# Optimization experiments

Hardware: AMD Instinct MI355X
Metric: run time of the kernel (lower is better)

The kernel has to match this reference:

```python
import jax, jax.numpy as jnp
import numpy as np

N_NODES = 100000
N_EDGES = 3200000
N_FEAT = 128
N_CLASSES = 8


def setup_inputs() -> dict:
    key = jax.random.key(0)
    ks = jax.random.split(key, 8)
    h = jax.random.normal(ks[0], (N_NODES, N_FEAT), dtype=jnp.float32)
    edge_index = jax.random.randint(ks[1], (2, N_EDGES), 0, N_NODES, dtype=jnp.int64)
    def lin(k, fi, fo):
        return jax.random.normal(k, (fi, fo), dtype=jnp.float32) / np.sqrt(fi)
    return {
        "h": h,
        "edge_index": edge_index,
        "W1": lin(ks[2], N_FEAT, 16), "b1": jnp.zeros((16,), jnp.float32),
        "W2": lin(ks[3], 16, 4),      "b2": jnp.zeros((4,), jnp.float32),
        "W3": lin(ks[4], 4, 2),      "b3": jnp.zeros((2,), jnp.float32),
        "Wc": lin(ks[5], 2, N_CLASSES), "bc": jnp.zeros((N_CLASSES,), jnp.float32),
    }


def _gcn_norm(edge_index, n_nodes):
    # PyG GCNConv: add self-loops, symmetric normalization deg^-1/2 A deg^-1/2
    loop = jnp.arange(n_nodes, dtype=edge_index.dtype)
    src = jnp.concatenate([edge_index[0], loop])  # [E+N]
    dst = jnp.concatenate([edge_index[1], loop])
    deg = jax.ops.segment_sum(jnp.ones_like(dst, dtype=jnp.float32), dst,
                              num_segments=n_nodes)
    dinv = jnp.where(deg > 0, jax.lax.rsqrt(deg), 0.0)
    norm = dinv[src] * dinv[dst]  # [E+N]
    return src, dst, norm


def _gcn_conv(x, W, b, src, dst, norm, n_nodes):
    xw = x @ W                                # [N, Fo] linear first (small Fo)
    msg = xw[src] * norm[:, None]             # gather + scale  [E+N, Fo]
    out = jax.ops.segment_sum(msg, dst, num_segments=n_nodes)  # scatter-add
    return out + b


def reference(h, edge_index, W1, b1, W2, b2, W3, b3, Wc, bc):
    n = h.shape[0]
    src, dst, norm = _gcn_norm(edge_index, n)
    h1 = jnp.tanh(_gcn_conv(h, W1, b1, src, dst, norm, n))
    h2 = jnp.tanh(_gcn_conv(h1, W2, b2, src, dst, norm, n))
    h3 = jnp.tanh(_gcn_conv(h2, W3, b3, src, dst, norm, n))
    out = h3 @ Wc + bc
    return (out, h3)
```

## Files before the change

### kernel.cpp

```cpp
#include <hip/hip_runtime.h>
#include <math.h>

#define N_NODES 100000
#define N_EDGES 3200000
#define NPB    256
#define NBUCK  ((N_NODES + NPB - 1) / NPB)
#define NBLKA  256
#define EPB    ((N_EDGES + NBLKA - 1) / NBLKA)
#define NB_BLK ((N_NODES + 255) / 256)

#define NEW_WS_WORDS (3u*N_NODES + N_EDGES + 3200000u + NBUCK*NBLKA + NBUCK + 2u)
#define NEW_WS_BYTES (NEW_WS_WORDS * 4u)
#define ATOMIC_WS_BYTES ((33u*N_NODES + 16u) * 4u)

__global__ void k_detect_i64(const int* __restrict__ ei_words, int* __restrict__ flag) {
    if (blockIdx.x == 0 && threadIdx.x == 0) {
        int allzero = 1;
        for (int i = 0; i < 64; i++)
            if (ei_words[2 * i + 1] != 0) allzero = 0;
        *flag = allzero;
    }
}

__device__ __forceinline__ unsigned load_idx(const int* p32, const long long* p64,
                                             int is64, int e) {
    return is64 ? (unsigned)(unsigned long long)p64[e] : (unsigned)p32[e];
}

__global__ __launch_bounds__(256) void k_bcount(const int* __restrict__ dst32,
                                                const long long* __restrict__ dst64,
                                                const int* __restrict__ flag,
                                                int* __restrict__ cmat) {
    __shared__ int lc[NBUCK];
    int t = threadIdx.x, blk = blockIdx.x;
    for (int i = t; i < NBUCK; i += 256) lc[i] = 0;
    __syncthreads();
    int is64 = *flag;
    int e0 = blk * EPB;
    int e1 = e0 + EPB; if (e1 > N_EDGES) e1 = N_EDGES;
    for (int e = e0 + t; e < e1; e += 256) {
        unsigned d = load_idx(dst32, dst64, is64, e);
        if (d < N_NODES) atomicAdd(&lc[d >> 8], 1);
    }
    __syncthreads();
    for (int b = t; b < NBUCK; b += 256) cmat[b * NBLKA + blk] = lc[b];
}

__global__ __launch_bounds__(256) void k_bsum(const int* __restrict__ cmat,
                                              int* __restrict__ bt) {
    int b = blockIdx.x, t = threadIdx.x;
    int v = cmat[b * NBLKA + t];
#pragma unroll
    for (int off = 32; off > 0; off >>= 1) v += __shfl_down(v, off, 64);
    __shared__ int s[4];
    if ((t & 63) == 0) s[t >> 6] = v;
    __syncthreads();
    if (t == 0) bt[b] = s[0] + s[1] + s[2] + s[3];
}

__global__ __launch_bounds__(512) void k_btscan(int* __restrict__ bt) {
    __shared__ int s[512];
    int t = threadIdx.x;
    s[t] = (t < NBUCK) ? bt[t] : 0;
    __syncthreads();
    for (int off = 1; off < 512; off <<= 1) {
        int v = (t >= off) ? s[t - off] : 0;
        __syncthreads();
        s[t] += v;
        __syncthreads();
    }
    if (t < NBUCK) bt[t] = (t == 0) ? 0 : s[t - 1];
    if (t == 0) bt[NBUCK] = s[NBUCK - 1];
}

__global__ __launch_bounds__(256) void k_boffs(int* __restrict__ cmat,
                                               const int* __restrict__ bt) {
    __shared__ int s[256];
    int b = blockIdx.x, t = threadIdx.x;
    int v0 = cmat[b * NBLKA + t];
    s[t] = v0;
    __syncthreads();
    for (int off = 1; off < 256; off <<= 1) {
        int v = (t >= off) ? s[t - off] : 0;
        __syncthreads();
        s[t] += v;
        __syncthreads();
    }
    cmat[b * NBLKA + t] = ((t == 0) ? 0 : s[t - 1]) + bt[b];
}

__global__ __launch_bounds__(256) void k_bscatter(const int* __restrict__ src32,
                                                  const long long* __restrict__ src64,
                                                  const int* __restrict__ dst32,
                                                  const long long* __restrict__ dst64,
                                                  const int* __restrict__ flag,
                                                  const int* __restrict__ cmat,
                                                  int* __restrict__ P) {
    __shared__ int cur[NBUCK];
    int t = threadIdx.x, blk = blockIdx.x;
    for (int i = t; i < NBUCK; i += 256) cur[i] = cmat[i * NBLKA + blk];
    __syncthreads();
    int is64 = *flag;
    int e0 = blk * EPB;
    int e1 = e0 + EPB; if (e1 > N_EDGES) e1 = N_EDGES;
    for (int e = e0 + t; e < e1; e += 256) {
        unsigned d = load_idx(dst32, dst64, is64, e);
        if (d < N_NODES) {
            unsigned s = load_idx(src32, src64, is64, e);
            int pos = atomicAdd(&cur[d >> 8], 1);
            P[pos] = (int)(((d & 255u) << 17) | (s & 0x1FFFFu));
        }
    }
}

__global__ __launch_bounds__(256) void k_bbuild(const int* __restrict__ P,
                                                const int* __restrict__ bt,
                                                int* __restrict__ adj,
                                                int* __restrict__ rowstart,
                                                int* __restrict__ rowend,
                                                float* __restrict__ dinv) {
    __shared__ int cnt[NPB];
    __shared__ int s[NPB];
    int b = blockIdx.x, t = threadIdx.x;
    int bo = bt[b], be = bt[b + 1];
    cnt[t] = 0;
    __syncthreads();
    for (int i = bo + t; i < be; i += 256) atomicAdd(&cnt[P[i] >> 17], 1);
    __syncthreads();
    s[t] = cnt[t];
    __syncthreads();
    for (int off = 1; off < 256; off <<= 1) {
        int v = (t >= off) ? s[t - off] : 0;
        __syncthreads();
        s[t] += v;
        __syncthreads();
    }
    int ex = (t == 0) ? 0 : s[t - 1];
    int node = b * NPB + t;
    if (node < N_NODES) {
        rowstart[node] = bo + ex;
        rowend[node]   = bo + ex + cnt[t];
        dinv[node]     = rsqrtf((float)cnt[t] + 1.0f);
    }
    __syncthreads();
    s[t] = ex;
    __syncthreads();
    for (int i = bo + t; i < be; i += 256) {
        int ent = P[i];
        int pos = bo + atomicAdd(&s[ent >> 17], 1);
        adj[pos] = ent & 0x1FFFF;
    }
}

__global__ __launch_bounds__(256) void k_gemm1(const float* __restrict__ h,
                                               const float* __restrict__ W,
                                               const float* __restrict__ dinv,
                                               float* __restrict__ xs,
                                               float* acc) {
    __shared__ float Wt[16 * 132];
    __shared__ float Hs[16 * 132];
    int tid = threadIdx.x;
    for (int i = tid; i < 2048; i += 256) {
        int k = i >> 4, f = i & 15;
        Wt[f * 132 + k] = W[i];
    }
    int nodeBase = blockIdx.x * 16;
    for (int i = tid; i < 512; i += 256) {
        int r = i >> 5, c = i & 31;
        float4 v = ((const float4*)(h + (size_t)(nodeBase + r) * 128))[c];
        *((float4*)&Hs[r * 132 + c * 4]) = v;
    }
    __syncthreads();
    int nl = tid >> 4;
    int f  = tid & 15;
    int n  = nodeBase + nl;
    const float* hr = &Hs[nl * 132];
    const float* wr = &Wt[f * 132];
    float s = 0.0f;
#pragma unroll
    for (int k = 0; k < 128; k++) s += hr[k] * wr[k];
    s *= dinv[n];
    xs[n * 16 + f]  = s;
    acc[n * 16 + f] = s;
}

template <int FI, int FO>
__global__ __launch_bounds__(256) void k_gemm_small(const float* __restrict__ x,
                                                    const float* __restrict__ W,
                                                    const float* __restrict__ dinv,
                                                    float* __restrict__ xs,
                                                    float* acc) {
    int i = blockIdx.x * 256 + threadIdx.x;
    if (i >= N_NODES * FO) return;
    int n = i / FO, f = i % FO;
    float s = 0.0f;
#pragma unroll
    for (int k = 0; k < FI; k++) s += x[n * FI + k] * W[k * FO + f];
    s *= dinv[n];
    xs[i] = s;
    acc[i] = s;
}

template <int F, int NL>
__global__ __launch_bounds__(256) void k_pull(const float* __restrict__ xs,
                                              const int* __restrict__ adj,
                                              const int* __restrict__ rowstart,
                                              const int* __restrict__ rowend,
                                              const float* __restrict__ dinv,
                                              const float* __restrict__ b,
                                              float* __restrict__ out) {
    constexpr int R = NL / F;
    int t = threadIdx.x;
    int g = t / NL, q = t % NL;
    int f = q % F,  k = q / F;
    int n = blockIdx.x * (256 / NL) + g;
    if (n >= N_NODES) return;
    int s0 = rowstart[n], e0 = rowend[n];
    float acc = 0.0f;
    for (int j = s0 + k; j < e0; j += R)
        acc += xs[adj[j] * F + f];
#pragma unroll
    for (int off = NL / 2; off >= F; off >>= 1)
        acc += __shfl_xor(acc, off, 64);
    if (k == 0) {
        acc += xs[n * F + f];
        out[n * F + f] = tanhf(dinv[n] * acc + b[f]);
    }
}

__global__ __launch_bounds__(256) void k_pull_final(const float* __restrict__ xs,
                                                    const int* __restrict__ adj,
                                                    const int* __restrict__ rowstart,
                                                    const int* __restrict__ rowend,
                                                    const float* __restrict__ dinv,
                                                    const float* __restrict__ b3,
                                                    const float* __restrict__ Wc,
                                                    const float* __restrict__ bc,
                                                    float* __restrict__ out,
                                                    float* __restrict__ h3out) {
    const int NL = 8;
    int t = threadIdx.x;
    int g = t / NL, q = t % NL;
    int f = q & 1, k = q >> 1;
    int n = blockIdx.x * (256 / NL) + g;
    if (n >= N_NODES) return;
    int s0 = rowstart[n], e0 = rowend[n];
    float acc = 0.0f;
    for (int j = s0 + k; j < e0; j += 4)
        acc += xs[adj[j] * 2 + f];
    acc += __shfl_xor(acc, 4, 64);
    acc += __shfl_xor(acc, 2, 64);
    float a = 0.0f;
    if (q < 2) {
        acc += xs[n * 2 + f];
        a = tanhf(dinv[n] * acc + b3[f]);
        h3out[2 * n + f] = a;
    }
    int wl = t & 63, gb = wl & ~7;
    float a0 = __shfl(a, gb, 64);
    float a1 = __shfl(a, gb + 1, 64);
    out[8 * n + q] = a0 * Wc[q] + a1 * Wc[8 + q] + bc[q];
}

template <int F>
__global__ __launch_bounds__(256) void k_scatter(const int* __restrict__ src32,
                                                 const long long* __restrict__ src64,
                                                 const int* __restrict__ dst32,
                                                 const long long* __restrict__ dst64,
                                                 const int* __restrict__ flag,
                                                 const float* __restrict__ xs,
                                                 float* __restrict__ acc) {
    long long gid = (long long)blockIdx.x * 256 + threadIdx.x;
    int e = (int)(gid / F), f = (int)(gid % F);
    if (e < N_EDGES) {
        int is64 = *flag;
        unsigned s = load_idx(src32, src64, is64, e);
        unsigned d = load_idx(dst32, dst64, is64, e);
        if (s < N_NODES && d < N_NODES)
            atomicAdd(&acc[d * F + f], xs[s * F + f]);
    }
}
__global__ __launch_bounds__(256) void k_deg_init(float* __restrict__ deg) {
    int i = blockIdx.x * 256 + threadIdx.x;
    if (i < N_NODES) deg[i] = 1.0f;
}
__global__ __launch_bounds__(256) void k_deg_count(const int* __restrict__ dst32,
                                                   const long long* __restrict__ dst64,
                                                   const int* __restrict__ flag,
                                                   float* __restrict__ deg) {
    int e = blockIdx.x * 256 + threadIdx.x;
    if (e < N_EDGES) {
        unsigned d = load_idx(dst32, dst64, *flag, e);
        if (d < N_NODES) atomicAdd(&deg[d], 1.0f);
    }
}
__global__ __launch_bounds__(256) void k_rsqrt(float* __restrict__ deg) {
    int i = blockIdx.x * 256 + threadIdx.x;
    if (i < N_NODES) deg[i] = rsqrtf(deg[i]);
}
template <int F>
__global__ __launch_bounds__(256) void k_finish(const float* __restrict__ acc,
                                                const float* __restrict__ dinv,
                                                const float* __restrict__ b,
                                                float* __restrict__ out) {
    int i = blockIdx.x * 256 + threadIdx.x;
    if (i >= N_NODES * F) return;
    int n = i / F, f = i % F;
    out[i] = tanhf(dinv[n] * acc[i] + b[f]);
}
__global__ __launch_bounds__(256) void k_final(const float* __restrict__ acc3,
                                               const float* __restrict__ dinv,
                                               const float* __restrict__ b3,
                                               const float* __restrict__ Wc,
                                               const float* __restrict__ bc,
                                               float* __restrict__ out,
                                               float* __restrict__ h3out) {
    int n = blockIdx.x * 256 + threadIdx.x;
    if (n >= N_NODES) return;
    float di = dinv[n];
    float a0 = tanhf(di * acc3[2 * n + 0] + b3[0]);
    float a1 = tanhf(di * acc3[2 * n + 1] + b3[1]);
    h3out[2 * n + 0] = a0;
    h3out[2 * n + 1] = a1;
#pragma unroll
    for (int c = 0; c < 8; c++)
        out[8 * n + c] = a0 * Wc[c] + a1 * Wc[8 + c] + bc[c];
}
__global__ __launch_bounds__(256) void k_zero_out(float* __restrict__ out, int n) {
    int i = blockIdx.x * 256 + threadIdx.x;
    if (i < n) out[i] = 0.0f;
}

extern "C" void kernel_launch(void* const* d_in, const int* in_sizes, int n_in,
                              void* d_out, int out_size, void* d_ws, size_t ws_size,
                              hipStream_t stream) {
    float* out = (float*)d_out;
    const float* h   = (const float*)d_in[0];
    const void*  ei  = d_in[1];
    const float* W1  = (const float*)d_in[2];
    const float* b1  = (const float*)d_in[3];
    const float* W2  = (const float*)d_in[4];
    const float* b2  = (const float*)d_in[5];
    const float* W3  = (const float*)d_in[6];
    const float* b3  = (const float*)d_in[7];
    const float* Wc  = (const float*)d_in[8];
    const float* bc  = (const float*)d_in[9];

    const int*       src32 = (const int*)ei;
    const int*       dst32 = src32 + N_EDGES;
    const long long* src64 = (const long long*)ei;
    const long long* dst64 = src64 + N_EDGES;

    float* h3out = out + 8 * N_NODES;
    const int NB_E = (N_EDGES + 255) / 256;

    if (d_ws != nullptr && ws_size >= NEW_WS_BYTES) {
        float* dinv    = (float*)d_ws;
        int* rowstart  = (int*)(dinv + N_NODES);
        int* rowend    = rowstart + N_NODES;
        int* adj       = rowend + N_NODES;
        int* S         = adj + N_EDGES;
        float* xs      = (float*)S;
        float* hbuf    = xs + 16 * N_NODES;
        int* P         = S;
        int* cmat      = S + 3200000;
        int* bt        = cmat + NBUCK * NBLKA;
        int* flag      = bt + NBUCK + 1;

        k_detect_i64<<<1, 64, 0, stream>>>(src32, flag);
        k_bcount<<<NBLKA, 256, 0, stream>>>(dst32, dst64, flag, cmat);
        k_bsum<<<NBUCK, 256, 0, stream>>>(cmat, bt);
        k_btscan<<<1, 512, 0, stream>>>(bt);
        k_boffs<<<NBUCK, 256, 0, stream>>>(cmat, bt);
        k_bscatter<<<NBLKA, 256, 0, stream>>>(src32, src64, dst32, dst64, flag, cmat, P);
        k_bbuild<<<NBUCK, 256, 0, stream>>>(P, bt, adj, rowstart, rowend, dinv);

        k_gemm1<<<N_NODES / 16, 256, 0, stream>>>(h, W1, dinv, xs, xs);
        k_pull<16, 64><<<(N_NODES * 64 + 255) / 256, 256, 0, stream>>>(
            xs, adj, rowstart, rowend, dinv, b1, hbuf);
        k_gemm_small<16, 4><<<(N_NODES * 4 + 255) / 256, 256, 0, stream>>>(hbuf, W2, dinv, xs, xs);
        k_pull<4, 16><<<(N_NODES * 16 + 255) / 256, 256, 0, stream>>>(
            xs, adj, rowstart, rowend, dinv, b2, hbuf);
        k_gemm_small<4, 2><<<(N_NODES * 2 + 255) / 256, 256, 0, stream>>>(hbuf, W3, dinv, xs, xs);
        k_pull_final<<<(N_NODES * 8 + 255) / 256, 256, 0, stream>>>(
            xs, adj, rowstart, rowend, dinv, b3, Wc, bc, out, h3out);
        return;
    }

    if (d_ws != nullptr && ws_size >= ATOMIC_WS_BYTES) {
        float* ws   = (float*)d_ws;
        float* dinv = ws;
        float* bufA = dinv + N_NODES;
        float* bufB = bufA + 16 * N_NODES;
        int*   flag = (int*)(bufB + 16 * N_NODES);
        float* xs1 = bufA, *acc1 = bufB, *h1 = bufA;
        float* xs2 = bufB, *acc2 = bufB + 4 * N_NODES, *h2 = bufA;
        float* xs3 = bufB, *acc3 = bufB + 2 * N_NODES;

        k_detect_i64<<<1, 64, 0, stream>>>(src32, flag);
        k_deg_init<<<NB_BLK, 256, 0, stream>>>(dinv);
        k_deg_count<<<NB_E, 256, 0, stream>>>(dst32, dst64, flag, dinv);
        k_rsqrt<<<NB_BLK, 256, 0, stream>>>(dinv);
        k_gemm1<<<N_NODES / 16, 256, 0, stream>>>(h, W1, dinv, xs1, acc1);
        k_scatter<16><<<(int)(((long long)N_EDGES * 16 + 255) / 256), 256, 0, stream>>>(
            src32, src64, dst32, dst64, flag, xs1, acc1);
        k_finish<16><<<(N_NODES * 16 + 255) / 256, 256, 0, stream>>>(acc1, dinv, b1, h1);
        k_gemm_small<16, 4><<<(N_NODES * 4 + 255) / 256, 256, 0, stream>>>(h1, W2, dinv, xs2, acc2);
        k_scatter<4><<<(int)(((long long)N_EDGES * 4 + 255) / 256), 256, 0, stream>>>(
            src32, src64, dst32, dst64, flag, xs2, acc2);
        k_finish<4><<<(N_NODES * 4 + 255) / 256, 256, 0, stream>>>(acc2, dinv, b2, h2);
        k_gemm_small<4, 2><<<(N_NODES * 2 + 255) / 256, 256, 0, stream>>>(h2, W3, dinv, xs3, acc3);
        k_scatter<2><<<(int)(((long long)N_EDGES * 2 + 255) / 256), 256, 0, stream>>>(
            src32, src64, dst32, dst64, flag, xs3, acc3);
        k_final<<<NB_BLK, 256, 0, stream>>>(acc3, dinv, b3, Wc, bc, out, h3out);
        return;
    }

    k_zero_out<<<(out_size + 255) / 256, 256, 0, stream>>>(out, out_size);
}
```

Baseline: 351.0 us.

## Split layer-1 features into two 8-wide halves, add nontemporal loads, double bucket blocks

Layer-1 features are stored as two planar 8-wide halves, and each half is aggregated in its own pull pass so the gather working set per pass is smaller and more cache-friendly. The layer-2 pull moves from 16 to 32 lanes per node. Nontemporal loads are used for edge indices, P, adj and h to avoid polluting cache with streamed data. The bucket-sort block count doubles to 512, and the scan kernels are adjusted to match. The split means adj is read twice for layer 1, and the extra pull launch adds overhead.

```diff
diff --git a/kernel.cpp b/kernel.cpp
--- a/kernel.cpp
+++ b/kernel.cpp
@@ -5,12 +5,14 @@
 #define N_EDGES 3200000
 #define NPB    256
 #define NBUCK  ((N_NODES + NPB - 1) / NPB)
-#define NBLKA  256
+#define NBLKA  512
 #define EPB    ((N_EDGES + NBLKA - 1) / NBLKA)
 #define NB_BLK ((N_NODES + 255) / 256)
 
-#define NEW_WS_WORDS (3u*N_NODES + N_EDGES + 3200000u + NBUCK*NBLKA + NBUCK + 2u)
-#define NEW_WS_BYTES (NEW_WS_WORDS * 4u)
+typedef float f4nt __attribute__((ext_vector_type(4)));
+
+#define MAIN_WS_WORDS (3u*N_NODES + N_EDGES + 3200000u + NBUCK*NBLKA + NBUCK + 2u)
+#define MAIN_WS_BYTES (MAIN_WS_WORDS * 4u)
 #define ATOMIC_WS_BYTES ((33u*N_NODES + 16u) * 4u)
 
 __global__ void k_detect_i64(const int* __restrict__ ei_words, int* __restrict__ flag) {
@@ -24,7 +26,8 @@
 
 __device__ __forceinline__ unsigned load_idx(const int* p32, const long long* p64,
                                              int is64, int e) {
-    return is64 ? (unsigned)(unsigned long long)p64[e] : (unsigned)p32[e];
+    return is64 ? (unsigned)(unsigned long long)__builtin_nontemporal_load(&p64[e])
+                : (unsigned)__builtin_nontemporal_load(&p32[e]);
 }
 
 __global__ __launch_bounds__(256) void k_bcount(const int* __restrict__ dst32,
@@ -36,8 +39,7 @@
     for (int i = t; i < NBUCK; i += 256) lc[i] = 0;
     __syncthreads();
     int is64 = *flag;
-    int e0 = blk * EPB;
-    int e1 = e0 + EPB; if (e1 > N_EDGES) e1 = N_EDGES;
+    int e0 = blk * EPB, e1 = e0 + EPB; if (e1 > N_EDGES) e1 = N_EDGES;
     for (int e = e0 + t; e < e1; e += 256) {
         unsigned d = load_idx(dst32, dst64, is64, e);
         if (d < N_NODES) atomicAdd(&lc[d >> 8], 1);
@@ -49,7 +51,7 @@
 __global__ __launch_bounds__(256) void k_bsum(const int* __restrict__ cmat,
                                               int* __restrict__ bt) {
     int b = blockIdx.x, t = threadIdx.x;
-    int v = cmat[b * NBLKA + t];
+    int v = cmat[b * NBLKA + t] + cmat[b * NBLKA + t + 256];
 #pragma unroll
     for (int off = 32; off > 0; off >>= 1) v += __shfl_down(v, off, 64);
     __shared__ int s[4];
@@ -73,14 +75,13 @@
     if (t == 0) bt[NBUCK] = s[NBUCK - 1];
 }
 
-__global__ __launch_bounds__(256) void k_boffs(int* __restrict__ cmat,
+__global__ __launch_bounds__(512) void k_boffs(int* __restrict__ cmat,
                                                const int* __restrict__ bt) {
-    __shared__ int s[256];
+    __shared__ int s[512];
     int b = blockIdx.x, t = threadIdx.x;
-    int v0 = cmat[b * NBLKA + t];
-    s[t] = v0;
-    __syncthreads();
-    for (int off = 1; off < 256; off <<= 1) {
+    s[t] = cmat[b * NBLKA + t];
+    __syncthreads();
+    for (int off = 1; off < 512; off <<= 1) {
         int v = (t >= off) ? s[t - off] : 0;
         __syncthreads();
         s[t] += v;
@@ -101,8 +102,7 @@
     for (int i = t; i < NBUCK; i += 256) cur[i] = cmat[i * NBLKA + blk];
     __syncthreads();
     int is64 = *flag;
-    int e0 = blk * EPB;
-    int e1 = e0 + EPB; if (e1 > N_EDGES) e1 = N_EDGES;
+    int e0 = blk * EPB, e1 = e0 + EPB; if (e1 > N_EDGES) e1 = N_EDGES;
     for (int e = e0 + t; e < e1; e += 256) {
         unsigned d = load_idx(dst32, dst64, is64, e);
         if (d < N_NODES) {
@@ -125,7 +125,8 @@
     int bo = bt[b], be = bt[b + 1];
     cnt[t] = 0;
     __syncthreads();
-    for (int i = bo + t; i < be; i += 256) atomicAdd(&cnt[P[i] >> 17], 1);
+    for (int i = bo + t; i < be; i += 256)
+        atomicAdd(&cnt[__builtin_nontemporal_load(&P[i]) >> 17], 1);
     __syncthreads();
     s[t] = cnt[t];
     __syncthreads();
@@ -146,17 +147,16 @@
     s[t] = ex;
     __syncthreads();
     for (int i = bo + t; i < be; i += 256) {
-        int ent = P[i];
+        int ent = __builtin_nontemporal_load(&P[i]);
         int pos = bo + atomicAdd(&s[ent >> 17], 1);
         adj[pos] = ent & 0x1FFFF;
     }
 }
 
-__global__ __launch_bounds__(256) void k_gemm1(const float* __restrict__ h,
-                                               const float* __restrict__ W,
-                                               const float* __restrict__ dinv,
-                                               float* __restrict__ xs,
-                                               float* acc) {
+__global__ __launch_bounds__(256) void k_gemm1_p(const float* __restrict__ h,
+                                                 const float* __restrict__ W,
+                                                 const float* __restrict__ dinv,
+                                                 float* __restrict__ xs) {
     __shared__ float Wt[16 * 132];
     __shared__ float Hs[16 * 132];
     int tid = threadIdx.x;
@@ -167,68 +167,64 @@
     int nodeBase = blockIdx.x * 16;
     for (int i = tid; i < 512; i += 256) {
         int r = i >> 5, c = i & 31;
-        float4 v = ((const float4*)(h + (size_t)(nodeBase + r) * 128))[c];
-        *((float4*)&Hs[r * 132 + c * 4]) = v;
-    }
-    __syncthreads();
-    int nl = tid >> 4;
-    int f  = tid & 15;
-    int n  = nodeBase + nl;
+        f4nt v = __builtin_nontemporal_load(
+            ((const f4nt*)(h + (size_t)(nodeBase + r) * 128)) + c);
+        *((f4nt*)&Hs[r * 132 + c * 4]) = v;
+    }
+    __syncthreads();
+    int nl = tid >> 4, f = tid & 15;
+    int n = nodeBase + nl;
     const float* hr = &Hs[nl * 132];
     const float* wr = &Wt[f * 132];
     float s = 0.0f;
 #pragma unroll
     for (int k = 0; k < 128; k++) s += hr[k] * wr[k];
     s *= dinv[n];
-    xs[n * 16 + f]  = s;
-    acc[n * 16 + f] = s;
+    xs[(f >> 3) * (8 * N_NODES) + n * 8 + (f & 7)] = s;
 }
 
 template <int FI, int FO>
-__global__ __launch_bounds__(256) void k_gemm_small(const float* __restrict__ x,
-                                                    const float* __restrict__ W,
-                                                    const float* __restrict__ dinv,
-                                                    float* __restrict__ xs,
-                                                    float* acc) {
+__global__ __launch_bounds__(256) void k_gemm_smallp(const float* __restrict__ x,
+                                                     const float* __restrict__ W,
+                                                     const float* __restrict__ dinv,
+                                                     float* __restrict__ xs) {
     int i = blockIdx.x * 256 + threadIdx.x;
     if (i >= N_NODES * FO) return;
     int n = i / FO, f = i % FO;
     float s = 0.0f;
 #pragma unroll
     for (int k = 0; k < FI; k++) s += x[n * FI + k] * W[k * FO + f];
-    s *= dinv[n];
-    xs[i] = s;
-    acc[i] = s;
-}
-
-template <int F, int NL>
-__global__ __launch_bounds__(256) void k_pull(const float* __restrict__ xs,
+    xs[i] = s * dinv[n];
+}
+
+template <int F, int NL, int FTOT, int FOFF>
+__global__ __launch_bounds__(256) void k_pull(const float* __restrict__ xsp,
                                               const int* __restrict__ adj,
                                               const int* __restrict__ rowstart,
                                               const int* __restrict__ rowend,
                                               const float* __restrict__ dinv,
-                                              const float* __restrict__ b,
+                                              const float* __restrict__ bias,
                                               float* __restrict__ out) {
     constexpr int R = NL / F;
     int t = threadIdx.x;
     int g = t / NL, q = t % NL;
-    int f = q % F,  k = q / F;
+    int f = q % F, k = q / F;
     int n = blockIdx.x * (256 / NL) + g;
     if (n >= N_NODES) return;
     int s0 = rowstart[n], e0 = rowend[n];
     float acc = 0.0f;
     for (int j = s0 + k; j < e0; j += R)
-        acc += xs[adj[j] * F + f];
+        acc += xsp[__builtin_nontemporal_load(&adj[j]) * F + f];
 #pragma unroll
     for (int off = NL / 2; off >= F; off >>= 1)
         acc += __shfl_xor(acc, off, 64);
     if (k == 0) {
-        acc += xs[n * F + f];
-        out[n * F + f] = tanhf(dinv[n] * acc + b[f]);
-    }
-}
-
-__global__ __launch_bounds__(256) void k_pull_final(const float* __restrict__ xs,
+        acc += xsp[n * F + f];
+        out[n * FTOT + FOFF + f] = tanhf(dinv[n] * acc + bias[f]);
+    }
+}
+
+__global__ __launch_bounds__(256) void k_pull_final(const float* __restrict__ xsp,
                                                     const int* __restrict__ adj,
                                                     const int* __restrict__ rowstart,
                                                     const int* __restrict__ rowend,
@@ -247,12 +243,12 @@
     int s0 = rowstart[n], e0 = rowend[n];
     float acc = 0.0f;
     for (int j = s0 + k; j < e0; j += 4)
-        acc += xs[adj[j] * 2 + f];
+        acc += xsp[__builtin_nontemporal_load(&adj[j]) * 2 + f];
     acc += __shfl_xor(acc, 4, 64);
     acc += __shfl_xor(acc, 2, 64);
     float a = 0.0f;
     if (q < 2) {
-        acc += xs[n * 2 + f];
+        acc += xsp[n * 2 + f];
         a = tanhf(dinv[n] * acc + b3[f]);
         h3out[2 * n + f] = a;
     }
@@ -262,6 +258,50 @@
     out[8 * n + q] = a0 * Wc[q] + a1 * Wc[8 + q] + bc[q];
 }
 
+__global__ __launch_bounds__(256) void k_gemm1(const float* __restrict__ h,
+                                               const float* __restrict__ W,
+                                               const float* __restrict__ dinv,
+                                               float* __restrict__ xs, float* acc) {
+    __shared__ float Wt[16 * 132];
+    __shared__ float Hs[16 * 132];
+    int tid = threadIdx.x;
+    for (int i = tid; i < 2048; i += 256) {
+        int k = i >> 4, f = i & 15;
+        Wt[f * 132 + k] = W[i];
+    }
+    int nodeBase = blockIdx.x * 16;
+    for (int i = tid; i < 512; i += 256) {
+        int r = i >> 5, c = i & 31;
+        float4 v = ((const float4*)(h + (size_t)(nodeBase + r) * 128))[c];
+        *((float4*)&Hs[r * 132 + c * 4]) = v;
+    }
+    __syncthreads();
+    int nl = tid >> 4, f = tid & 15;
+    int n = nodeBase + nl;
+    const float* hr = &Hs[nl * 132];
+    const float* wr = &Wt[f * 132];
+    float s = 0.0f;
+#pragma unroll
+    for (int k = 0; k < 128; k++) s += hr[k] * wr[k];
+    s *= dinv[n];
+    xs[n * 16 + f] = s;
+    acc[n * 16 + f] = s;
+}
+template <int FI, int FO>
+__global__ __launch_bounds__(256) void k_gemm_small(const float* __restrict__ x,
+                                                    const float* __restrict__ W,
+                                                    const float* __restrict__ dinv,
+                                                    float* __restrict__ xs, float* acc) {
+    int i = blockIdx.x * 256 + threadIdx.x;
+    if (i >= N_NODES * FO) return;
+    int n = i / FO, f = i % FO;
+    float s = 0.0f;
+#pragma unroll
+    for (int k = 0; k < FI; k++) s += x[n * FI + k] * W[k * FO + f];
+    s *= dinv[n];
+    xs[i] = s;
+    acc[i] = s;
+}
 template <int F>
 __global__ __launch_bounds__(256) void k_scatter(const int* __restrict__ src32,
                                                  const long long* __restrict__ src64,
@@ -354,35 +394,37 @@
     float* h3out = out + 8 * N_NODES;
     const int NB_E = (N_EDGES + 255) / 256;
 
-    if (d_ws != nullptr && ws_size >= NEW_WS_BYTES) {
-        float* dinv    = (float*)d_ws;
-        int* rowstart  = (int*)(dinv + N_NODES);
-        int* rowend    = rowstart + N_NODES;
-        int* adj       = rowend + N_NODES;
-        int* S         = adj + N_EDGES;
-        float* xs      = (float*)S;
-        float* hbuf    = xs + 16 * N_NODES;
-        int* P         = S;
-        int* cmat      = S + 3200000;
-        int* bt        = cmat + NBUCK * NBLKA;
-        int* flag      = bt + NBUCK + 1;
+    if (d_ws != nullptr && ws_size >= MAIN_WS_BYTES) {
+        float* dinv   = (float*)d_ws;
+        int* rowstart = (int*)(dinv + N_NODES);
+        int* rowend   = rowstart + N_NODES;
+        int* adj      = rowend + N_NODES;
+        int* S        = adj + N_EDGES;
+        float* xs     = (float*)S;
+        float* hbuf   = xs + 16 * N_NODES;
+        int* P        = S;
+        int* cmat     = S + 3200000;
+        int* bt       = cmat + NBUCK * NBLKA;
+        int* flag     = bt + NBUCK + 1;
 
         k_detect_i64<<<1, 64, 0, stream>>>(src32, flag);
         k_bcount<<<NBLKA, 256, 0, stream>>>(dst32, dst64, flag, cmat);
         k_bsum<<<NBUCK, 256, 0, stream>>>(cmat, bt);
         k_btscan<<<1, 512, 0, stream>>>(bt);
-        k_boffs<<<NBUCK, 256, 0, stream>>>(cmat, bt);
+        k_boffs<<<NBUCK, 512, 0, stream>>>(cmat, bt);
         k_bscatter<<<NBLKA, 256, 0, stream>>>(src32, src64, dst32, dst64, flag, cmat, P);
         k_bbuild<<<NBUCK, 256, 0, stream>>>(P, bt, adj, rowstart, rowend, dinv);
 
-        k_gemm1<<<N_NODES / 16, 256, 0, stream>>>(h, W1, dinv, xs, xs);
-        k_pull<16, 64><<<(N_NODES * 64 + 255) / 256, 256, 0, stream>>>(
+        k_gemm1_p<<<N_NODES / 16, 256, 0, stream>>>(h, W1, dinv, xs);
+        k_pull<8, 64, 16, 0><<<25000, 256, 0, stream>>>(
             xs, adj, rowstart, rowend, dinv, b1, hbuf);
-        k_gemm_small<16, 4><<<(N_NODES * 4 + 255) / 256, 256, 0, stream>>>(hbuf, W2, dinv, xs, xs);
-        k_pull<4, 16><<<(N_NODES * 16 + 255) / 256, 256, 0, stream>>>(
+        k_pull<8, 64, 16, 8><<<25000, 256, 0, stream>>>(
+            xs + 8 * N_NODES, adj, rowstart, rowend, dinv, b1 + 8, hbuf);
+        k_gemm_smallp<16, 4><<<(N_NODES * 4 + 255) / 256, 256, 0, stream>>>(hbuf, W2, dinv, xs);
+        k_pull<4, 32, 4, 0><<<12500, 256, 0, stream>>>(
             xs, adj, rowstart, rowend, dinv, b2, hbuf);
-        k_gemm_small<4, 2><<<(N_NODES * 2 + 255) / 256, 256, 0, stream>>>(hbuf, W3, dinv, xs, xs);
-        k_pull_final<<<(N_NODES * 8 + 255) / 256, 256, 0, stream>>>(
+        k_gemm_smallp<4, 2><<<(N_NODES * 2 + 255) / 256, 256, 0, stream>>>(hbuf, W3, dinv, xs);
+        k_pull_final<<<3125, 256, 0, stream>>>(
             xs, adj, rowstart, rowend, dinv, b3, Wc, bc, out, h3out);
         return;
     }
```

After: 435.6 us. +24.1%, slower.
